# Kernel tuning notes

Measured on AMD Instinct MI355X. Metric: run time of the kernel, lower is better.

## Reference

```python
import jax, jax.numpy as jnp
import numpy as np

N_NODES = 100000
N_EDGES = 1600000
N_GRAPHS = 1024
F = 128
L = 3  # num_gnn_layers
EPS = 1e-5


def _ln(x, g, b):
    mu = jnp.mean(x, axis=-1, keepdims=True)
    v = jnp.mean((x - mu) ** 2, axis=-1, keepdims=True)
    return (x - mu) * jax.lax.rsqrt(v + EPS) * g + b


def setup_inputs() -> dict:
    key = jax.random.key(0)
    ks = jax.random.split(key, 40)
    s = 0.05
    d = {}
    d['x'] = jax.random.normal(ks[0], (N_NODES, F), jnp.float32)
    d['w'] = jax.random.uniform(ks[1], (N_NODES, 1), jnp.float32)
    d['edge_index'] = jax.random.randint(ks[2], (2, N_EDGES), 0, N_NODES)
    d['batch'] = jnp.sort(jax.random.randint(ks[3], (N_NODES,), 0, N_GRAPHS))
    # input linear: (monomer_features+1) -> gc_features
    d['W_in'] = jax.random.normal(ks[4], (F + 1, F), jnp.float32) * s
    d['b_in'] = jnp.zeros((F,), jnp.float32)
    # stacked GCBlock params [L, ...]
    d['sage_Wl'] = jax.random.normal(ks[5], (L, F, F), jnp.float32) * s
    d['sage_bl'] = jnp.zeros((L, F), jnp.float32)
    d['sage_Wr'] = jax.random.normal(ks[6], (L, F, F), jnp.float32) * s
    d['ln1_g'] = jnp.ones((L, F), jnp.float32)
    d['ln1_b'] = jnp.zeros((L, F), jnp.float32)
    d['lin1_W'] = jax.random.normal(ks[7], (L, F, F), jnp.float32) * s
    d['lin1_b'] = jnp.zeros((L, F), jnp.float32)
    d['lin2_W'] = jax.random.normal(ks[8], (L, F, F), jnp.float32) * s
    d['lin2_b'] = jnp.zeros((L, F), jnp.float32)
    d['ln2_g'] = jnp.ones((L, F), jnp.float32)
    d['ln2_b'] = jnp.zeros((L, F), jnp.float32)
    # MeanDiffFeatureBlock: Linear(2F -> F)
    d['mdf_W'] = jax.random.normal(ks[9], (2 * F, F), jnp.float32) * s
    d['mdf_b'] = jnp.zeros((F,), jnp.float32)
    # mean PoolingLayer params
    d['pln1_g'] = jnp.ones((F,), jnp.float32)
    d['pln1_b'] = jnp.zeros((F,), jnp.float32)
    d['plin1_W'] = jax.random.normal(ks[10], (F, F), jnp.float32) * s
    d['plin1_b'] = jnp.zeros((F,), jnp.float32)
    d['plin2_W'] = jax.random.normal(ks[11], (F, F), jnp.float32) * s
    d['plin2_b'] = jnp.zeros((F,), jnp.float32)
    d['pln2_g'] = jnp.ones((F,), jnp.float32)
    d['pln2_b'] = jnp.zeros((F,), jnp.float32)
    return d


def reference(x, w, edge_index, batch, W_in, b_in, sage_Wl, sage_bl, sage_Wr,
              ln1_g, ln1_b, lin1_W, lin1_b, lin2_W, lin2_b, ln2_g, ln2_b,
              mdf_W, mdf_b, pln1_g, pln1_b, plin1_W, plin1_b, plin2_W, plin2_b,
              pln2_g, pln2_b):
    src, dst = edge_index[0], edge_index[1]
    # in-degree for SAGE mean aggregation (clamped so isolated nodes -> 0 agg)
    deg = jax.ops.segment_sum(jnp.ones((N_EDGES,), jnp.float32), dst,
                              num_segments=N_NODES)
    deg = jnp.maximum(deg, 1.0)[:, None]
    # graph sizes for global_mean_pool
    cnt = jax.ops.segment_sum(jnp.ones((N_NODES,), jnp.float32), batch,
                              num_segments=N_GRAPHS)
    cnt = jnp.maximum(cnt, 1.0)[:, None]

    # inilinear on [x, weight-fraction]  (scalers are identity at init)
    h = jnp.concatenate([x, w], axis=-1) @ W_in + b_in  # [N, F]

    def gc_block(h, p):
        Wl, bl, Wr, g1, b1, W1, bb1, W2, bb2, g2, b2 = p
        # SAGEConv: lin_l(mean_j x_j) + lin_r(x_i)
        agg = jax.ops.segment_sum(h[src], dst, num_segments=N_NODES) / deg
        y = agg @ Wl + bl + h @ Wr
        y1 = _ln(y + h, g1, b1)
        y2 = jax.nn.elu(y1 @ W1 + bb1) @ W2 + bb2  # dropout = identity (eval)
        return _ln(y2 + y1, g2, b2), None

    h, _ = jax.lax.scan(gc_block, h,
                        (sage_Wl, sage_bl, sage_Wr, ln1_g, ln1_b,
                         lin1_W, lin1_b, lin2_W, lin2_b, ln2_g, ln2_b))

    # MeanDiffFeatureBlock
    gm = jax.ops.segment_sum(h, batch, num_segments=N_GRAPHS) / cnt  # [B, F]
    h = jnp.concatenate([h, h - gm[batch]], axis=-1) @ mdf_W + mdf_b

    # mean PoolingLayer
    p = jax.ops.segment_sum(h, batch, num_segments=N_GRAPHS) / cnt  # [B, F]
    hh = _ln(p, pln1_g, pln1_b)
    y = jax.nn.elu(hh @ plin1_W + plin1_b) @ plin2_W + plin2_b
    return _ln(y + hh, pln2_g, pln2_b)  # [B, F]
```

## Files before the change

### kernel.cpp

```cpp
#include <hip/hip_runtime.h>
#include <math.h>

#define NN 100000
#define NE 1600000
#define NG 1024
#define FF 128
#define BSH 9
#define NBK ((NN + 511) >> BSH)
#define RB 512
#define BCAP 16384

typedef __attribute__((ext_vector_type(8))) short short8;
typedef __attribute__((ext_vector_type(4))) float f32x4;
typedef __attribute__((ext_vector_type(2))) float f32x2;

__device__ __forceinline__ unsigned short f2b(float f) {
    union { float f; unsigned u; } v; v.f = f;
    unsigned r = (v.u + 0x7FFF + ((v.u >> 16) & 1)) >> 16;
    return (unsigned short)r;
}
__device__ __forceinline__ float us2f(unsigned short u) {
    union { unsigned u; float f; } v; v.u = ((unsigned)u) << 16; return v.f;
}
__device__ __forceinline__ float fast_elu(float v) {
    float e = __builtin_amdgcn_exp2f(v * 1.44269504088896340736f) - 1.0f;
    return v > 0.f ? v : e;
}
__device__ __forceinline__ uint2 pk8(const float* v) {
    unsigned lo = 0, hi = 0;
    lo = (unsigned)__builtin_amdgcn_cvt_pk_fp8_f32(v[0], v[1], (int)lo, false);
    lo = (unsigned)__builtin_amdgcn_cvt_pk_fp8_f32(v[2], v[3], (int)lo, true);
    hi = (unsigned)__builtin_amdgcn_cvt_pk_fp8_f32(v[4], v[5], (int)hi, false);
    hi = (unsigned)__builtin_amdgcn_cvt_pk_fp8_f32(v[6], v[7], (int)hi, true);
    uint2 r; r.x = lo; r.y = hi; return r;
}
#define MFMA(a, b, c) __builtin_amdgcn_mfma_f32_16x16x32_bf16((a), (b), (c), 0, 0, 0)

__global__ __launch_bounds__(256)
void radix_scatter(const int* __restrict__ src, const int* __restrict__ dst,
                   int* __restrict__ bcur, unsigned* __restrict__ pairs, int n) {
    __shared__ int base[NBK];
    __shared__ int cnt[NBK];
    for (int i = threadIdx.x; i < NBK; i += 256) cnt[i] = 0;
    __syncthreads();
    const int per = (((n + RB - 1) / RB) + 3) & ~3;
    const int beg = blockIdx.x * per;
    const int end = min(n, beg + per);
    {
        int i = beg + 4 * (int)threadIdx.x;
        for (; i + 3 < end; i += 1024) {
            int4 d4 = *(const int4*)&dst[i];
            atomicAdd(&cnt[d4.x >> BSH], 1);
            atomicAdd(&cnt[d4.y >> BSH], 1);
            atomicAdd(&cnt[d4.z >> BSH], 1);
            atomicAdd(&cnt[d4.w >> BSH], 1);
        }
        for (; i < end; ++i) atomicAdd(&cnt[dst[i] >> BSH], 1);
    }
    __syncthreads();
    for (int i = threadIdx.x; i < NBK; i += 256)
        base[i] = cnt[i] ? atomicAdd(&bcur[i], cnt[i]) : 0;
    __syncthreads();
    {
        int i = beg + 4 * (int)threadIdx.x;
        for (; i + 3 < end; i += 1024) {
            int4 d4 = *(const int4*)&dst[i];
            int4 s4 = *(const int4*)&src[i];
            int p;
            p = atomicAdd(&base[d4.x >> BSH], 1);
            pairs[p] = ((unsigned)s4.x << BSH) | (unsigned)(d4.x & 511);
            p = atomicAdd(&base[d4.y >> BSH], 1);
            pairs[p] = ((unsigned)s4.y << BSH) | (unsigned)(d4.y & 511);
            p = atomicAdd(&base[d4.z >> BSH], 1);
            pairs[p] = ((unsigned)s4.z << BSH) | (unsigned)(d4.z & 511);
            p = atomicAdd(&base[d4.w >> BSH], 1);
            pairs[p] = ((unsigned)s4.w << BSH) | (unsigned)(d4.w & 511);
        }
        for (; i < end; ++i) {
            int d = dst[i];
            int p = atomicAdd(&base[d >> BSH], 1);
            pairs[p] = ((unsigned)src[i] << BSH) | (unsigned)(d & 511);
        }
    }
}

__global__ __launch_bounds__(512)
void bucket_build(const unsigned* __restrict__ pairs, const int* __restrict__ bcur,
                  int* __restrict__ row_beg, int* __restrict__ row_end,
                  float* __restrict__ inv_deg, int* __restrict__ ssrc,
                  const int* __restrict__ batch, int* __restrict__ g_off,
                  float* __restrict__ inv_cnt) {
    __shared__ int cnt[512];
    __shared__ int curs[512];
    __shared__ int wsum[8];
    const int b = blockIdx.x;
    const int n0 = b << BSH;
    const int t = threadIdx.x;
    const int lane = t & 63, wid = t >> 6;

    {
        int g = b * 512 + t;
        if (g <= NG) {
            if (g == NG) {
                g_off[NG] = NN;
            } else {
                int lo = 0, hi = NN;
                while (lo < hi) { int mid = (lo + hi) >> 1; if (batch[mid] < g) lo = mid + 1; else hi = mid; }
                int lo2 = lo, hi2 = NN;
                while (lo2 < hi2) { int mid = (lo2 + hi2) >> 1; if (batch[mid] < g + 1) lo2 = mid + 1; else hi2 = mid; }
                g_off[g] = lo;
                int c = lo2 - lo;
                inv_cnt[g] = 1.0f / (float)(c > 1 ? c : 1);
            }
        }
    }

    cnt[t] = 0;
    __syncthreads();
    const int beg = b * BCAP, end = bcur[b];
    {
        int i = beg + 4 * t;
        for (; i + 3 < end; i += 2048) {
            uint4 p4 = *(const uint4*)&pairs[i];
            atomicAdd(&cnt[p4.x & 511], 1);
            atomicAdd(&cnt[p4.y & 511], 1);
            atomicAdd(&cnt[p4.z & 511], 1);
            atomicAdd(&cnt[p4.w & 511], 1);
        }
        for (; i < end; ++i) atomicAdd(&cnt[pairs[i] & 511], 1);
    }
    __syncthreads();

    int c = cnt[t];
    int x = c;
    #pragma unroll
    for (int o = 1; o < 64; o <<= 1) {
        int y = __shfl_up(x, o);
        if (lane >= o) x += y;
    }
    if (lane == 63) wsum[wid] = x;
    __syncthreads();
    if (t == 0) {
        int s = 0;
        #pragma unroll
        for (int w2 = 0; w2 < 8; ++w2) { int tv = wsum[w2]; wsum[w2] = s; s += tv; }
    }
    __syncthreads();
    int g0 = beg + wsum[wid] + x - c;
    curs[t] = g0;
    {
        int node = n0 + t;
        if (node < NN) {
            row_beg[node] = g0; row_end[node] = g0 + c;
            inv_deg[node] = 1.0f / (float)(c > 1 ? c : 1);
        }
    }
    __syncthreads();
    {
        int i = beg + 4 * t;
        for (; i + 3 < end; i += 2048) {
            uint4 p4 = *(const uint4*)&pairs[i];
            int p;
            p = atomicAdd(&curs[p4.x & 511], 1); ssrc[p] = (int)(p4.x >> BSH) << 7;
            p = atomicAdd(&curs[p4.y & 511], 1); ssrc[p] = (int)(p4.y >> BSH) << 7;
            p = atomicAdd(&curs[p4.z & 511], 1); ssrc[p] = (int)(p4.z >> BSH) << 7;
            p = atomicAdd(&curs[p4.w & 511], 1); ssrc[p] = (int)(p4.w >> BSH) << 7;
        }
        for (; i < end; ++i) {
            unsigned pr = pairs[i];
            int p = atomicAdd(&curs[pr & 511], 1);
            ssrc[p] = (int)(pr >> BSH) << 7;
        }
    }
}

struct WTab { const float* a[16]; };
__global__ __launch_bounds__(256)
void prep_weights(WTab tab, unsigned short* __restrict__ dst,
                  int* __restrict__ bcur, int* __restrict__ ssrc) {
    __shared__ unsigned short Wl[128 * 128];
    const int w = blockIdx.x;
    const int t = threadIdx.x;
    if (w == 0) {
        for (int i = t; i < NBK; i += 256) bcur[i] = i * BCAP;
        if (t == 0) ssrc[0] = 0;
    }
    const float4* src = (const float4*)tab.a[w];
    for (int i = t; i < 4096; i += 256) {
        float4 v = src[i];
        ushort4 o = {f2b(v.x), f2b(v.y), f2b(v.z), f2b(v.w)};
        *(ushort4*)&Wl[i * 4] = o;
    }
    __syncthreads();
    unsigned short* dw = dst + (size_t)w * 16384;
    for (int i2 = 0; i2 < 64; ++i2) {
        int idx = t + i2 * 256;
        int j = idx & 7, lane = (idx >> 3) & 63, nt = (idx >> 9) & 7, kc = idx >> 12;
        int cb = lane & 15, rq = lane >> 4;
        int k = kc * 32 + rq * 8 + j;
        int n = nt * 16 + cb;
        dw[idx] = Wl[k * 128 + n];
    }
}

__global__ __launch_bounds__(256)
void sage_agg(const unsigned char* __restrict__ h8, const int* __restrict__ row_beg,
              const int* __restrict__ row_end, const float* __restrict__ inv_deg,
              const int* __restrict__ ssrc, unsigned short* __restrict__ aggb) {
    const int wid = threadIdx.x >> 6;
    const int lane = threadIdx.x & 63;
    const int n0 = blockIdx.x * 8 + wid * 2;
    const int n1 = n0 + 1;
    const int eg = lane >> 4, j = lane & 15;
    const int jo = j * 8;
    const int beg0 = row_beg[n0], end0 = row_end[n0];
    const int beg1 = row_beg[n1], end1 = row_end[n1];
    f32x2 a0 = {0.f, 0.f}, a1 = {0.f, 0.f}, a2 = {0.f, 0.f}, a3 = {0.f, 0.f};
    f32x2 b0 = {0.f, 0.f}, b1 = {0.f, 0.f}, b2 = {0.f, 0.f}, b3 = {0.f, 0.f};
    int e0 = beg0 + eg, e1 = beg1 + eg;
    const int d0 = end0 - beg0, d1 = end1 - beg1;
    const int nit = ((d0 > d1 ? d0 : d1) + 31) >> 5;
    for (int it = 0; it < nit; ++it, e0 += 32, e1 += 32) {
        uint2 u0[8], u1[8];
        #pragma unroll
        for (int k = 0; k < 8; ++k) {
            int ek = e0 + 4 * k;
            bool ok = ek < end0;
            int idx = ssrc[ok ? ek : 0];
            uint2 uu = *(const uint2*)(h8 + (unsigned)(idx + jo));
            uu.x = ok ? uu.x : 0u;
            uu.y = ok ? uu.y : 0u;
            u0[k] = uu;
        }
        #pragma unroll
        for (int k = 0; k < 8; ++k) {
            int ek = e1 + 4 * k;
            bool ok = ek < end1;
            int idx = ssrc[ok ? ek : 0];
            uint2 uu = *(const uint2*)(h8 + (unsigned)(idx + jo));
            uu.x = ok ? uu.x : 0u;
            uu.y = ok ? uu.y : 0u;
            u1[k] = uu;
        }
        #pragma unroll
        for (int k = 0; k < 8; ++k) {
            a0 += __builtin_amdgcn_cvt_pk_f32_fp8(u0[k].x, false);
            a1 += __builtin_amdgcn_cvt_pk_f32_fp8(u0[k].x, true);
            a2 += __builtin_amdgcn_cvt_pk_f32_fp8(u0[k].y, false);
            a3 += __builtin_amdgcn_cvt_pk_f32_fp8(u0[k].y, true);
            b0 += __builtin_amdgcn_cvt_pk_f32_fp8(u1[k].x, false);
            b1 += __builtin_amdgcn_cvt_pk_f32_fp8(u1[k].x, true);
            b2 += __builtin_amdgcn_cvt_pk_f32_fp8(u1[k].y, false);
            b3 += __builtin_amdgcn_cvt_pk_f32_fp8(u1[k].y, true);
        }
    }
    float af[8] = {a0.x, a0.y, a1.x, a1.y, a2.x, a2.y, a3.x, a3.y};
    float bf[8] = {b0.x, b0.y, b1.x, b1.y, b2.x, b2.y, b3.x, b3.y};
    #pragma unroll
    for (int k = 0; k < 8; ++k) {
        af[k] += __shfl_xor(af[k], 16);
        af[k] += __shfl_xor(af[k], 32);
        bf[k] += __shfl_xor(bf[k], 16);
        bf[k] += __shfl_xor(bf[k], 32);
    }
    if (eg == 0) {
        float id0 = inv_deg[n0];
        float id1 = inv_deg[n1];
        #pragma unroll
        for (int nt = 0; nt < 8; ++nt) {
            aggb[(size_t)n0 * 128 + nt * 16 + j] = f2b(af[nt] * id0);
            aggb[(size_t)n1 * 128 + nt * 16 + j] = f2b(bf[nt] * id1);
        }
    }
}

__global__ __launch_bounds__(256)
void pool_mean_b(const unsigned short* __restrict__ src, const int* __restrict__ g_off,
                 const float* __restrict__ inv_cnt, float* __restrict__ out) {
    __shared__ float red[3][128];
    const int g = blockIdx.x;
    const int t = threadIdx.x;
    const int lane = t & 63, wid = t >> 6;
    const int j = lane & 15, rs = lane >> 4;
    const int beg = g_off[g], end = g_off[g + 1];
    float s[8] = {0.f, 0.f, 0.f, 0.f, 0.f, 0.f, 0.f, 0.f};
    for (int n = beg + rs + wid * 4; n < end; n += 16) {
        short8 v = *(const short8*)&src[(size_t)n * FF + j * 8];
        #pragma unroll
        for (int i = 0; i < 8; ++i) s[i] += us2f((unsigned short)v[i]);
    }
    #pragma unroll
    for (int i = 0; i < 8; ++i) {
        s[i] += __shfl_xor(s[i], 16);
        s[i] += __shfl_xor(s[i], 32);
    }
    if (wid > 0 && rs == 0) {
        #pragma unroll
        for (int i = 0; i < 8; ++i) red[wid - 1][j * 8 + i] = s[i];
    }
    __syncthreads();
    if (wid == 0 && rs == 0) {
        float ic = inv_cnt[g];
        #pragma unroll
        for (int i = 0; i < 8; ++i) {
            float v = s[i] + red[0][j * 8 + i] + red[1][j * 8 + i] + red[2][j * 8 + i];
            out[(size_t)g * FF + j * 8 + i] = v * ic;
        }
    }
}

template<bool AB16, bool R1, int RESM, int ACT, bool LN, bool OF32, bool OB16, bool OB8>
__global__ __launch_bounds__(256)
void gemm_mfma(const void* __restrict__ A_,
               const unsigned short* __restrict__ Wf,
               const float* __restrict__ bias,
               const float* __restrict__ rvec, const float* __restrict__ rrow,
               const float* __restrict__ res,
               const float* __restrict__ lng, const float* __restrict__ lnb,
               float* __restrict__ outf, unsigned short* __restrict__ outb,
               unsigned char* __restrict__ outb8, int M) {
    __shared__ short Al[64 * 136];

    const int t = threadIdx.x;
    const int lane = t & 63, wid = t >> 6;
    const int m0 = blockIdx.x * 64;
    const int cb = lane & 15, rq = lane >> 4;
    const int band = wid * 16;

    if (AB16) {
        const unsigned short* Ab = (const unsigned short*)A_;
        #pragma unroll
        for (int i2 = 0; i2 < 4; ++i2) {
            int i = lane + i2 * 64;
            int row = band + (i >> 4), seg = i & 15;
            int gr = m0 + row; if (gr >= M) gr = M - 1;
            *(uint4*)&Al[row * 136 + seg * 8] = *(const uint4*)&Ab[(size_t)gr * 128 + seg * 8];
        }
    } else {
        const float* Af = (const float*)A_;
        #pragma unroll
        for (int i2 = 0; i2 < 8; ++i2) {
            int i = lane + i2 * 64;
            int row = band + (i >> 5), seg = i & 31;
            int gr = m0 + row; if (gr >= M) gr = M - 1;
            float4 v = *(const float4*)&Af[(size_t)gr * 128 + seg * 4];
            ushort4 o = {f2b(v.x), f2b(v.y), f2b(v.z), f2b(v.w)};
            *(ushort4*)&Al[row * 136 + seg * 4] = o;
        }
    }

    f32x4 acc[8];
    #pragma unroll
    for (int nt = 0; nt < 8; ++nt) acc[nt] = (f32x4){0.f, 0.f, 0.f, 0.f};

    const int aoff_base = (band + cb) * 136 + rq * 8;
    for (int kc = 0; kc < 4; ++kc) {
        short8 a0 = *(const short8*)&Al[aoff_base + kc * 32];
        #pragma unroll
        for (int nt = 0; nt < 8; ++nt) {
            short8 b0 = *(const short8*)&Wf[(size_t)(kc * 8 + nt) * 512 + lane * 8];
            acc[nt] = MFMA(a0, b0, acc[nt]);
        }
    }

    float bs[8], rr[8], lg[8], lb[8];
    #pragma unroll
    for (int nt = 0; nt < 8; ++nt) {
        int col = nt * 16 + cb;
        bs[nt] = bias[col];
        if (R1) rr[nt] = rrow[col];
        if (LN) { lg[nt] = lng[col]; lb[nt] = lnb[col]; }
    }
    #pragma unroll
    for (int reg = 0; reg < 4; ++reg) {
        int m = m0 + band + rq * 4 + reg;
        int mc = m < M ? m : M - 1;
        float v[8];
        #pragma unroll
        for (int nt = 0; nt < 8; ++nt) v[nt] = acc[nt][reg] + bs[nt];
        if (R1) {
            float rv = rvec[mc];
            #pragma unroll
            for (int nt = 0; nt < 8; ++nt) v[nt] += rv * rr[nt];
        }
        if (RESM == 1) {
            #pragma unroll
            for (int nt = 0; nt < 8; ++nt) v[nt] += res[(size_t)mc * 128 + nt * 16 + cb];
        }
        if (ACT == 1) {
            #pragma unroll
            for (int nt = 0; nt < 8; ++nt) v[nt] = fast_elu(v[nt]);
        }
        if (LN) {
            float s1 = 0.f, s2 = 0.f;
            #pragma unroll
            for (int nt = 0; nt < 8; ++nt) { s1 += v[nt]; s2 += v[nt] * v[nt]; }
            #pragma unroll
            for (int o = 8; o >= 1; o >>= 1) { s1 += __shfl_xor(s1, o); s2 += __shfl_xor(s2, o); }
            float mu = s1 * (1.f / 128.f);
            float rs = rsqrtf(s2 * (1.f / 128.f) - mu * mu + 1e-5f);
            #pragma unroll
            for (int nt = 0; nt < 8; ++nt) v[nt] = (v[nt] - mu) * rs * lg[nt] + lb[nt];
        }
        if (m < M) {
            #pragma unroll
            for (int nt = 0; nt < 8; ++nt) {
                size_t o = (size_t)m * 128 + nt * 16 + cb;
                if (OF32) outf[o] = v[nt];
                if (OB16) outb[o] = f2b(v[nt]);
            }
            if (OB8) *(uint2*)&outb8[(size_t)m * 128 + cb * 8] = pk8(v);
        }
    }
}

__global__ __launch_bounds__(256)
void gc_chain(const unsigned short* __restrict__ hin, const unsigned short* __restrict__ aggb,
              unsigned short* __restrict__ hout, unsigned char* __restrict__ h8out,
              const unsigned short* __restrict__ Wl_f, const unsigned short* __restrict__ Wr_f,
              const unsigned short* __restrict__ W1_f, const unsigned short* __restrict__ W2_f,
              const float* __restrict__ bl,
              const float* __restrict__ g1, const float* __restrict__ b1,
              const float* __restrict__ bb1, const float* __restrict__ bb2,
              const float* __restrict__ g2, const float* __restrict__ b2, int M) {
    __shared__ short Hl[64 * 136];
    __shared__ short Gl[64 * 136];

    const int t = threadIdx.x;
    const int lane = t & 63, wid = t >> 6;
    const int m0 = blockIdx.x * 64;
    const int cb = lane & 15, rq = lane >> 4;
    const int band = wid * 16;
    const int aoff_base = (band + cb) * 136 + rq * 8;
    const int boff = lane * 8;

    #pragma unroll
    for (int i2 = 0; i2 < 4; ++i2) {
        int i = lane + i2 * 64;
        int row = band + (i >> 4), seg = i & 15;
        int gr = m0 + row; if (gr >= M) gr = M - 1;
        *(uint4*)&Hl[row * 136 + seg * 8] = *(const uint4*)&hin[(size_t)gr * 128 + seg * 8];
        *(uint4*)&Gl[row * 136 + seg * 8] = *(const uint4*)&aggb[(size_t)gr * 128 + seg * 8];
    }

    f32x4 acc[8];
    #pragma unroll
    for (int nt = 0; nt < 8; ++nt) acc[nt] = (f32x4){0.f, 0.f, 0.f, 0.f};

    for (int kc = 0; kc < 4; ++kc) {
        short8 a0 = *(const short8*)&Gl[aoff_base + kc * 32];
        short8 a1 = *(const short8*)&Hl[aoff_base + kc * 32];
        #pragma unroll
        for (int nt = 0; nt < 8; ++nt) {
            const size_t wo = (size_t)(kc * 8 + nt) * 512 + boff;
            acc[nt] = MFMA(a0, *(const short8*)&Wl_f[wo], acc[nt]);
            acc[nt] = MFMA(a1, *(const short8*)&Wr_f[wo], acc[nt]);
        }
    }

    float y1r[4][8];
    {
        float bs[8], lg[8], lb[8];
        #pragma unroll
        for (int nt = 0; nt < 8; ++nt) {
            int col = nt * 16 + cb;
            bs[nt] = bl[col]; lg[nt] = g1[col]; lb[nt] = b1[col];
        }
        #pragma unroll
        for (int reg = 0; reg < 4; ++reg) {
            int r = band + rq * 4 + reg;
            float v[8];
            float s1 = 0.f, s2 = 0.f;
            #pragma unroll
            for (int nt = 0; nt < 8; ++nt) {
                v[nt] = acc[nt][reg] + bs[nt] + us2f((unsigned short)Hl[r * 136 + nt * 16 + cb]);
                s1 += v[nt]; s2 += v[nt] * v[nt];
            }
            #pragma unroll
            for (int o = 8; o >= 1; o >>= 1) { s1 += __shfl_xor(s1, o); s2 += __shfl_xor(s2, o); }
            float mu = s1 * (1.f / 128.f);
            float rs = rsqrtf(s2 * (1.f / 128.f) - mu * mu + 1e-5f);
            #pragma unroll
            for (int nt = 0; nt < 8; ++nt) {
                float y = (v[nt] - mu) * rs * lg[nt] + lb[nt];
                y1r[reg][nt] = y;
                Hl[r * 136 + nt * 16 + cb] = (short)f2b(y);
            }
        }
    }

    #pragma unroll
    for (int nt = 0; nt < 8; ++nt) acc[nt] = (f32x4){0.f, 0.f, 0.f, 0.f};
    for (int kc = 0; kc < 4; ++kc) {
        short8 a0 = *(const short8*)&Hl[aoff_base + kc * 32];
        #pragma unroll
        for (int nt = 0; nt < 8; ++nt)
            acc[nt] = MFMA(a0, *(const short8*)&W1_f[(size_t)(kc * 8 + nt) * 512 + boff], acc[nt]);
    }
    {
        float bs[8];
        #pragma unroll
        for (int nt = 0; nt < 8; ++nt) bs[nt] = bb1[nt * 16 + cb];
        #pragma unroll
        for (int reg = 0; reg < 4; ++reg) {
            int r = band + rq * 4 + reg;
            #pragma unroll
            for (int nt = 0; nt < 8; ++nt) {
                float v = fast_elu(acc[nt][reg] + bs[nt]);
                Gl[r * 136 + nt * 16 + cb] = (short)f2b(v);
            }
        }
    }

    #pragma unroll
    for (int nt = 0; nt < 8; ++nt) acc[nt] = (f32x4){0.f, 0.f, 0.f, 0.f};
    for (int kc = 0; kc < 4; ++kc) {
        short8 a0 = *(const short8*)&Gl[aoff_base + kc * 32];
        #pragma unroll
        for (int nt = 0; nt < 8; ++nt)
            acc[nt] = MFMA(a0, *(const short8*)&W2_f[(size_t)(kc * 8 + nt) * 512 + boff], acc[nt]);
    }
    {
        float bs[8], lg[8], lb[8];
        #pragma unroll
        for (int nt = 0; nt < 8; ++nt) {
            int col = nt * 16 + cb;
            bs[nt] = bb2[col]; lg[nt] = g2[col]; lb[nt] = b2[col];
        }
        #pragma unroll
        for (int reg = 0; reg < 4; ++reg) {
            int r = band + rq * 4 + reg;
            int m = m0 + r;
            float v[8];
            float s1 = 0.f, s2 = 0.f;
            #pragma unroll
            for (int nt = 0; nt < 8; ++nt) {
                v[nt] = acc[nt][reg] + bs[nt] + y1r[reg][nt];
                s1 += v[nt]; s2 += v[nt] * v[nt];
            }
            #pragma unroll
            for (int o = 8; o >= 1; o >>= 1) { s1 += __shfl_xor(s1, o); s2 += __shfl_xor(s2, o); }
            float mu = s1 * (1.f / 128.f);
            float rs = rsqrtf(s2 * (1.f / 128.f) - mu * mu + 1e-5f);
            if (m < M) {
                float fv[8];
                #pragma unroll
                for (int nt = 0; nt < 8; ++nt) {
                    fv[nt] = (v[nt] - mu) * rs * lg[nt] + lb[nt];
                    hout[(size_t)m * 128 + nt * 16 + cb] = f2b(fv[nt]);
                }
                *(uint2*)&h8out[(size_t)m * 128 + cb * 8] = pk8(fv);
            }
        }
    }
}

__global__ __launch_bounds__(256)
void head_chain(const float* __restrict__ gm,
                const unsigned short* __restrict__ Wa_f,
                const unsigned short* __restrict__ P1_f,
                const unsigned short* __restrict__ P2_f,
                const float* __restrict__ mdfb,
                const float* __restrict__ g1, const float* __restrict__ b1,
                const float* __restrict__ p1b, const float* __restrict__ p2b,
                const float* __restrict__ g2, const float* __restrict__ b2,
                float* __restrict__ outp) {
    __shared__ short Al[64 * 136];

    const int t = threadIdx.x;
    const int lane = t & 63, wid = t >> 6;
    const int m0 = blockIdx.x * 64;
    const int cb = lane & 15, rq = lane >> 4;
    const int band = wid * 16;
    const int aoff_base = (band + cb) * 136 + rq * 8;
    const int boff = lane * 8;

    #pragma unroll
    for (int i2 = 0; i2 < 8; ++i2) {
        int i = lane + i2 * 64;
        int row = band + (i >> 5), seg = i & 31;
        float4 v = *(const float4*)&gm[(size_t)(m0 + row) * 128 + seg * 4];
        ushort4 o = {f2b(v.x), f2b(v.y), f2b(v.z), f2b(v.w)};
        *(ushort4*)&Al[row * 136 + seg * 4] = o;
    }

    f32x4 acc[8];
    #pragma unroll
    for (int nt = 0; nt < 8; ++nt) acc[nt] = (f32x4){0.f, 0.f, 0.f, 0.f};
    for (int kc = 0; kc < 4; ++kc) {
        short8 a0 = *(const short8*)&Al[aoff_base + kc * 32];
        #pragma unroll
        for (int nt = 0; nt < 8; ++nt)
            acc[nt] = MFMA(a0, *(const short8*)&Wa_f[(size_t)(kc * 8 + nt) * 512 + boff], acc[nt]);
    }
    float y1r[4][8];
    {
        float bs[8], lg[8], lb[8];
        #pragma unroll
        for (int nt = 0; nt < 8; ++nt) {
            int col = nt * 16 + cb;
            bs[nt] = mdfb[col]; lg[nt] = g1[col]; lb[nt] = b1[col];
        }
        #pragma unroll
        for (int reg = 0; reg < 4; ++reg) {
            int r = band + rq * 4 + reg;
            float v[8];
            float s1 = 0.f, s2 = 0.f;
            #pragma unroll
            for (int nt = 0; nt < 8; ++nt) {
                v[nt] = acc[nt][reg] + bs[nt];
                s1 += v[nt]; s2 += v[nt] * v[nt];
            }
            #pragma unroll
            for (int o = 8; o >= 1; o >>= 1) { s1 += __shfl_xor(s1, o); s2 += __shfl_xor(s2, o); }
            float mu = s1 * (1.f / 128.f);
            float rs = rsqrtf(s2 * (1.f / 128.f) - mu * mu + 1e-5f);
            #pragma unroll
            for (int nt = 0; nt < 8; ++nt) {
                float y = (v[nt] - mu) * rs * lg[nt] + lb[nt];
                y1r[reg][nt] = y;
                Al[r * 136 + nt * 16 + cb] = (short)f2b(y);
            }
        }
    }

    #pragma unroll
    for (int nt = 0; nt < 8; ++nt) acc[nt] = (f32x4){0.f, 0.f, 0.f, 0.f};
    for (int kc = 0; kc < 4; ++kc) {
        short8 a0 = *(const short8*)&Al[aoff_base + kc * 32];
        #pragma unroll
        for (int nt = 0; nt < 8; ++nt)
            acc[nt] = MFMA(a0, *(const short8*)&P1_f[(size_t)(kc * 8 + nt) * 512 + boff], acc[nt]);
    }
    {
        float bs[8];
        #pragma unroll
        for (int nt = 0; nt < 8; ++nt) bs[nt] = p1b[nt * 16 + cb];
        #pragma unroll
        for (int reg = 0; reg < 4; ++reg) {
            int r = band + rq * 4 + reg;
            #pragma unroll
            for (int nt = 0; nt < 8; ++nt) {
                float v = fast_elu(acc[nt][reg] + bs[nt]);
                Al[r * 136 + nt * 16 + cb] = (short)f2b(v);
            }
        }
    }

    #pragma unroll
    for (int nt = 0; nt < 8; ++nt) acc[nt] = (f32x4){0.f, 0.f, 0.f, 0.f};
    for (int kc = 0; kc < 4; ++kc) {
        short8 a0 = *(const short8*)&Al[aoff_base + kc * 32];
        #pragma unroll
        for (int nt = 0; nt < 8; ++nt)
            acc[nt] = MFMA(a0, *(const short8*)&P2_f[(size_t)(kc * 8 + nt) * 512 + boff], acc[nt]);
    }
    {
        float bs[8], lg[8], lb[8];
        #pragma unroll
        for (int nt = 0; nt < 8; ++nt) {
            int col = nt * 16 + cb;
            bs[nt] = p2b[col]; lg[nt] = g2[col]; lb[nt] = b2[col];
        }
        #pragma unroll
        for (int reg = 0; reg < 4; ++reg) {
            int r = band + rq * 4 + reg;
            int m = m0 + r;
            float v[8];
            float s1 = 0.f, s2 = 0.f;
            #pragma unroll
            for (int nt = 0; nt < 8; ++nt) {
                v[nt] = acc[nt][reg] + bs[nt] + y1r[reg][nt];
                s1 += v[nt]; s2 += v[nt] * v[nt];
            }
            #pragma unroll
            for (int o = 8; o >= 1; o >>= 1) { s1 += __shfl_xor(s1, o); s2 += __shfl_xor(s2, o); }
            float mu = s1 * (1.f / 128.f);
            float rs = rsqrtf(s2 * (1.f / 128.f) - mu * mu + 1e-5f);
            #pragma unroll
            for (int nt = 0; nt < 8; ++nt)
                outp[(size_t)m * 128 + nt * 16 + cb] = (v[nt] - mu) * rs * lg[nt] + lb[nt];
        }
    }
}

extern "C" void kernel_launch(void* const* d_in, const int* in_sizes, int n_in,
                              void* d_out, int out_size, void* d_ws, size_t ws_size,
                              hipStream_t stream) {
    const float* x      = (const float*)d_in[0];
    const float* w      = (const float*)d_in[1];
    const int*   ei     = (const int*)d_in[2];
    const int*   batch  = (const int*)d_in[3];
    const float* W_in   = (const float*)d_in[4];
    const float* b_in   = (const float*)d_in[5];
    const float* sage_Wl = (const float*)d_in[6];
    const float* sage_bl = (const float*)d_in[7];
    const float* sage_Wr = (const float*)d_in[8];
    const float* ln1_g  = (const float*)d_in[9];
    const float* ln1_b  = (const float*)d_in[10];
    const float* lin1_W = (const float*)d_in[11];
    const float* lin1_b = (const float*)d_in[12];
    const float* lin2_W = (const float*)d_in[13];
    const float* lin2_b = (const float*)d_in[14];
    const float* ln2_g  = (const float*)d_in[15];
    const float* ln2_b  = (const float*)d_in[16];
    const float* mdf_W  = (const float*)d_in[17];
    const float* mdf_b  = (const float*)d_in[18];
    const float* pln1_g = (const float*)d_in[19];
    const float* pln1_b = (const float*)d_in[20];
    const float* plin1_W = (const float*)d_in[21];
    const float* plin1_b = (const float*)d_in[22];
    const float* plin2_W = (const float*)d_in[23];
    const float* plin2_b = (const float*)d_in[24];
    const float* pln2_g = (const float*)d_in[25];
    const float* pln2_b = (const float*)d_in[26];
    float* out = (float*)d_out;

    const int* e_src = ei;
    const int* e_dst = ei + NE;

    float* ws = (float*)d_ws;
    size_t off = 0;
    float* gm    = ws + off; off += (size_t)NG * FF;
    float* inv_deg = ws + off; off += NN;
    float* inv_cnt = ws + off; off += NG;
    unsigned short* us = (unsigned short*)(ws + off);
    size_t uoff = 0;
    unsigned short* hb0  = us + uoff; uoff += (size_t)NN * FF;
    unsigned short* hb1  = us + uoff; uoff += (size_t)NN * FF;
    unsigned short* aggb = us + uoff; uoff += (size_t)NN * FF;
    unsigned short* wt   = us + uoff; uoff += (size_t)16 * 16384;
    int* iw = (int*)(us + uoff);
    size_t ioff = 0;
    unsigned* pairs = (unsigned*)iw; ioff += (size_t)NBK * BCAP;
    int* ssrc    = iw + ioff; ioff += (size_t)NBK * BCAP;
    int* row_beg = iw + ioff; ioff += NN;
    int* row_end = iw + ioff; ioff += NN;
    int* g_off   = iw + ioff; ioff += NG + 1;
    int* bcur    = iw + ioff; ioff += NBK;
    unsigned char* h8 = (unsigned char*)pairs;

    WTab tab;
    tab.a[0] = W_in;
    for (int l = 0; l < 3; ++l) {
        tab.a[1 + l]  = sage_Wl + (size_t)l * 16384;
        tab.a[4 + l]  = sage_Wr + (size_t)l * 16384;
        tab.a[7 + l]  = lin1_W + (size_t)l * 16384;
        tab.a[10 + l] = lin2_W + (size_t)l * 16384;
    }
    tab.a[13] = mdf_W;
    tab.a[14] = plin1_W;
    tab.a[15] = plin2_W;
    prep_weights<<<16, 256, 0, stream>>>(tab, wt, bcur, ssrc);
    const unsigned short* win_t = wt + 0 * 16384;
    const unsigned short* wa_t  = wt + 13 * 16384;
    const unsigned short* p1_t  = wt + 14 * 16384;
    const unsigned short* p2_t  = wt + 15 * 16384;

    radix_scatter<<<RB, 256, 0, stream>>>(e_src, e_dst, bcur, pairs, NE);
    bucket_build<<<NBK, 512, 0, stream>>>(pairs, bcur, row_beg, row_end,
                                          inv_deg, ssrc, batch, g_off, inv_cnt);

    const int GN = (NN + 63) / 64;
    const int GB = NG / 64;

    gemm_mfma<false, true, 0, 0, false, false, true, true><<<GN, 256, 0, stream>>>(
        x, win_t, b_in, w, W_in + 128 * 128,
        nullptr, nullptr, nullptr, nullptr, hb0, h8, NN);

    unsigned short* hcur = hb0;
    unsigned short* hnxt = hb1;
    for (int l = 0; l < 3; ++l) {
        sage_agg<<<NN / 8, 256, 0, stream>>>(h8, row_beg, row_end, inv_deg, ssrc, aggb);
        gc_chain<<<GN, 256, 0, stream>>>(
            hcur, aggb, hnxt, h8,
            wt + (size_t)(1 + l) * 16384, wt + (size_t)(4 + l) * 16384,
            wt + (size_t)(7 + l) * 16384, wt + (size_t)(10 + l) * 16384,
            sage_bl + (size_t)l * FF,
            ln1_g + (size_t)l * FF, ln1_b + (size_t)l * FF,
            lin1_b + (size_t)l * FF, lin2_b + (size_t)l * FF,
            ln2_g + (size_t)l * FF, ln2_b + (size_t)l * FF, NN);
        unsigned short* tmp = hcur; hcur = hnxt; hnxt = tmp;
    }

    pool_mean_b<<<NG, 256, 0, stream>>>(hcur, g_off, inv_cnt, gm);
    head_chain<<<GB, 256, 0, stream>>>(
        gm, wa_t, p1_t, p2_t, mdf_b,
        pln1_g, pln1_b, plin1_b, plin2_b, pln2_g, pln2_b, out);
}
```

Baseline: 488.0 us.

## Fuse edge radix scatter with input GEMM in one launch; update h in place

Merges the edge radix-scatter kernel and the input linear GEMM into a single launch. The first RB blocks do the scatter and the remaining blocks do the GEMM, so the two independent stages run concurrently and one launch is removed. The fp8 copy of h moves out of the pairs buffer into its own region, since pairs is now still being written while the GEMM writes h8. gc_chain also reads and writes the same bf16 h buffer in place, dropping the ping-pong buffer. This relies on each block touching only its own rows.

```diff
diff --git a/kernel.cpp b/kernel.cpp
--- a/kernel.cpp
+++ b/kernel.cpp
@@ -37,49 +37,113 @@
 #define MFMA(a, b, c) __builtin_amdgcn_mfma_f32_16x16x32_bf16((a), (b), (c), 0, 0, 0)
 
 __global__ __launch_bounds__(256)
-void radix_scatter(const int* __restrict__ src, const int* __restrict__ dst,
-                   int* __restrict__ bcur, unsigned* __restrict__ pairs, int n) {
-    __shared__ int base[NBK];
-    __shared__ int cnt[NBK];
-    for (int i = threadIdx.x; i < NBK; i += 256) cnt[i] = 0;
-    __syncthreads();
-    const int per = (((n + RB - 1) / RB) + 3) & ~3;
-    const int beg = blockIdx.x * per;
-    const int end = min(n, beg + per);
-    {
-        int i = beg + 4 * (int)threadIdx.x;
-        for (; i + 3 < end; i += 1024) {
-            int4 d4 = *(const int4*)&dst[i];
-            atomicAdd(&cnt[d4.x >> BSH], 1);
-            atomicAdd(&cnt[d4.y >> BSH], 1);
-            atomicAdd(&cnt[d4.z >> BSH], 1);
-            atomicAdd(&cnt[d4.w >> BSH], 1);
-        }
-        for (; i < end; ++i) atomicAdd(&cnt[dst[i] >> BSH], 1);
-    }
-    __syncthreads();
-    for (int i = threadIdx.x; i < NBK; i += 256)
-        base[i] = cnt[i] ? atomicAdd(&bcur[i], cnt[i]) : 0;
-    __syncthreads();
-    {
-        int i = beg + 4 * (int)threadIdx.x;
-        for (; i + 3 < end; i += 1024) {
-            int4 d4 = *(const int4*)&dst[i];
-            int4 s4 = *(const int4*)&src[i];
-            int p;
-            p = atomicAdd(&base[d4.x >> BSH], 1);
-            pairs[p] = ((unsigned)s4.x << BSH) | (unsigned)(d4.x & 511);
-            p = atomicAdd(&base[d4.y >> BSH], 1);
-            pairs[p] = ((unsigned)s4.y << BSH) | (unsigned)(d4.y & 511);
-            p = atomicAdd(&base[d4.z >> BSH], 1);
-            pairs[p] = ((unsigned)s4.z << BSH) | (unsigned)(d4.z & 511);
-            p = atomicAdd(&base[d4.w >> BSH], 1);
-            pairs[p] = ((unsigned)s4.w << BSH) | (unsigned)(d4.w & 511);
-        }
-        for (; i < end; ++i) {
-            int d = dst[i];
-            int p = atomicAdd(&base[d >> BSH], 1);
-            pairs[p] = ((unsigned)src[i] << BSH) | (unsigned)(d & 511);
+void scatter_gemm(const int* __restrict__ src, const int* __restrict__ dst,
+                  int* __restrict__ bcur, unsigned* __restrict__ pairs, int n,
+                  const float* __restrict__ x, const unsigned short* __restrict__ Wf,
+                  const float* __restrict__ bias,
+                  const float* __restrict__ rvec, const float* __restrict__ rrow,
+                  unsigned short* __restrict__ outb, unsigned char* __restrict__ outb8,
+                  int M) {
+    __shared__ short Al[64 * 136];
+
+    if (blockIdx.x < RB) {
+        int* cnt  = (int*)Al;
+        int* base = cnt + NBK;
+        for (int i = threadIdx.x; i < NBK; i += 256) cnt[i] = 0;
+        __syncthreads();
+        const int per = (((n + RB - 1) / RB) + 3) & ~3;
+        const int beg = blockIdx.x * per;
+        const int end = min(n, beg + per);
+        {
+            int i = beg + 4 * (int)threadIdx.x;
+            for (; i + 3 < end; i += 1024) {
+                int4 d4 = *(const int4*)&dst[i];
+                atomicAdd(&cnt[d4.x >> BSH], 1);
+                atomicAdd(&cnt[d4.y >> BSH], 1);
+                atomicAdd(&cnt[d4.z >> BSH], 1);
+                atomicAdd(&cnt[d4.w >> BSH], 1);
+            }
+            for (; i < end; ++i) atomicAdd(&cnt[dst[i] >> BSH], 1);
+        }
+        __syncthreads();
+        for (int i = threadIdx.x; i < NBK; i += 256)
+            base[i] = cnt[i] ? atomicAdd(&bcur[i], cnt[i]) : 0;
+        __syncthreads();
+        {
+            int i = beg + 4 * (int)threadIdx.x;
+            for (; i + 3 < end; i += 1024) {
+                int4 d4 = *(const int4*)&dst[i];
+                int4 s4 = *(const int4*)&src[i];
+                int p;
+                p = atomicAdd(&base[d4.x >> BSH], 1);
+                pairs[p] = ((unsigned)s4.x << BSH) | (unsigned)(d4.x & 511);
+                p = atomicAdd(&base[d4.y >> BSH], 1);
+                pairs[p] = ((unsigned)s4.y << BSH) | (unsigned)(d4.y & 511);
+                p = atomicAdd(&base[d4.z >> BSH], 1);
+                pairs[p] = ((unsigned)s4.z << BSH) | (unsigned)(d4.z & 511);
+                p = atomicAdd(&base[d4.w >> BSH], 1);
+                pairs[p] = ((unsigned)s4.w << BSH) | (unsigned)(d4.w & 511);
+            }
+            for (; i < end; ++i) {
+                int d = dst[i];
+                int p = atomicAdd(&base[d >> BSH], 1);
+                pairs[p] = ((unsigned)src[i] << BSH) | (unsigned)(d & 511);
+            }
+        }
+        return;
+    }
+
+    const int bid = blockIdx.x - RB;
+    const int t = threadIdx.x;
+    const int lane = t & 63, wid = t >> 6;
+    const int m0 = bid * 64;
+    const int cb = lane & 15, rq = lane >> 4;
+    const int band = wid * 16;
+
+    #pragma unroll
+    for (int i2 = 0; i2 < 8; ++i2) {
+        int i = lane + i2 * 64;
+        int row = band + (i >> 5), seg = i & 31;
+        int gr = m0 + row; if (gr >= M) gr = M - 1;
+        float4 v = *(const float4*)&x[(size_t)gr * 128 + seg * 4];
+        ushort4 o = {f2b(v.x), f2b(v.y), f2b(v.z), f2b(v.w)};
+        *(ushort4*)&Al[row * 136 + seg * 4] = o;
+    }
+
+    f32x4 acc[8];
+    #pragma unroll
+    for (int nt = 0; nt < 8; ++nt) acc[nt] = (f32x4){0.f, 0.f, 0.f, 0.f};
+
+    const int aoff_base = (band + cb) * 136 + rq * 8;
+    for (int kc = 0; kc < 4; ++kc) {
+        short8 a0 = *(const short8*)&Al[aoff_base + kc * 32];
+        #pragma unroll
+        for (int nt = 0; nt < 8; ++nt) {
+            short8 b0 = *(const short8*)&Wf[(size_t)(kc * 8 + nt) * 512 + lane * 8];
+            acc[nt] = MFMA(a0, b0, acc[nt]);
+        }
+    }
+
+    float bs[8], rr[8];
+    #pragma unroll
+    for (int nt = 0; nt < 8; ++nt) {
+        int col = nt * 16 + cb;
+        bs[nt] = bias[col];
+        rr[nt] = rrow[col];
+    }
+    #pragma unroll
+    for (int reg = 0; reg < 4; ++reg) {
+        int m = m0 + band + rq * 4 + reg;
+        int mc = m < M ? m : M - 1;
+        float v[8];
+        float rv = rvec[mc];
+        #pragma unroll
+        for (int nt = 0; nt < 8; ++nt) v[nt] = acc[nt][reg] + bs[nt] + rv * rr[nt];
+        if (m < M) {
+            #pragma unroll
+            for (int nt = 0; nt < 8; ++nt)
+                outb[(size_t)m * 128 + nt * 16 + cb] = f2b(v[nt]);
+            *(uint2*)&outb8[(size_t)m * 128 + cb * 8] = pk8(v);
         }
     }
 }
@@ -309,114 +373,9 @@
     }
 }
 
-template<bool AB16, bool R1, int RESM, int ACT, bool LN, bool OF32, bool OB16, bool OB8>
 __global__ __launch_bounds__(256)
-void gemm_mfma(const void* __restrict__ A_,
-               const unsigned short* __restrict__ Wf,
-               const float* __restrict__ bias,
-               const float* __restrict__ rvec, const float* __restrict__ rrow,
-               const float* __restrict__ res,
-               const float* __restrict__ lng, const float* __restrict__ lnb,
-               float* __restrict__ outf, unsigned short* __restrict__ outb,
-               unsigned char* __restrict__ outb8, int M) {
-    __shared__ short Al[64 * 136];
-
-    const int t = threadIdx.x;
-    const int lane = t & 63, wid = t >> 6;
-    const int m0 = blockIdx.x * 64;
-    const int cb = lane & 15, rq = lane >> 4;
-    const int band = wid * 16;
-
-    if (AB16) {
-        const unsigned short* Ab = (const unsigned short*)A_;
-        #pragma unroll
-        for (int i2 = 0; i2 < 4; ++i2) {
-            int i = lane + i2 * 64;
-            int row = band + (i >> 4), seg = i & 15;
-            int gr = m0 + row; if (gr >= M) gr = M - 1;
-            *(uint4*)&Al[row * 136 + seg * 8] = *(const uint4*)&Ab[(size_t)gr * 128 + seg * 8];
-        }
-    } else {
-        const float* Af = (const float*)A_;
-        #pragma unroll
-        for (int i2 = 0; i2 < 8; ++i2) {
-            int i = lane + i2 * 64;
-            int row = band + (i >> 5), seg = i & 31;
-            int gr = m0 + row; if (gr >= M) gr = M - 1;
-            float4 v = *(const float4*)&Af[(size_t)gr * 128 + seg * 4];
-            ushort4 o = {f2b(v.x), f2b(v.y), f2b(v.z), f2b(v.w)};
-            *(ushort4*)&Al[row * 136 + seg * 4] = o;
-        }
-    }
-
-    f32x4 acc[8];
-    #pragma unroll
-    for (int nt = 0; nt < 8; ++nt) acc[nt] = (f32x4){0.f, 0.f, 0.f, 0.f};
-
-    const int aoff_base = (band + cb) * 136 + rq * 8;
-    for (int kc = 0; kc < 4; ++kc) {
-        short8 a0 = *(const short8*)&Al[aoff_base + kc * 32];
-        #pragma unroll
-        for (int nt = 0; nt < 8; ++nt) {
-            short8 b0 = *(const short8*)&Wf[(size_t)(kc * 8 + nt) * 512 + lane * 8];
-            acc[nt] = MFMA(a0, b0, acc[nt]);
-        }
-    }
-
-    float bs[8], rr[8], lg[8], lb[8];
-    #pragma unroll
-    for (int nt = 0; nt < 8; ++nt) {
-        int col = nt * 16 + cb;
-        bs[nt] = bias[col];
-        if (R1) rr[nt] = rrow[col];
-        if (LN) { lg[nt] = lng[col]; lb[nt] = lnb[col]; }
-    }
-    #pragma unroll
-    for (int reg = 0; reg < 4; ++reg) {
-        int m = m0 + band + rq * 4 + reg;
-        int mc = m < M ? m : M - 1;
-        float v[8];
-        #pragma unroll
-        for (int nt = 0; nt < 8; ++nt) v[nt] = acc[nt][reg] + bs[nt];
-        if (R1) {
-            float rv = rvec[mc];
-            #pragma unroll
-            for (int nt = 0; nt < 8; ++nt) v[nt] += rv * rr[nt];
-        }
-        if (RESM == 1) {
-            #pragma unroll
-            for (int nt = 0; nt < 8; ++nt) v[nt] += res[(size_t)mc * 128 + nt * 16 + cb];
-        }
-        if (ACT == 1) {
-            #pragma unroll
-            for (int nt = 0; nt < 8; ++nt) v[nt] = fast_elu(v[nt]);
-        }
-        if (LN) {
-            float s1 = 0.f, s2 = 0.f;
-            #pragma unroll
-            for (int nt = 0; nt < 8; ++nt) { s1 += v[nt]; s2 += v[nt] * v[nt]; }
-            #pragma unroll
-            for (int o = 8; o >= 1; o >>= 1) { s1 += __shfl_xor(s1, o); s2 += __shfl_xor(s2, o); }
-            float mu = s1 * (1.f / 128.f);
-            float rs = rsqrtf(s2 * (1.f / 128.f) - mu * mu + 1e-5f);
-            #pragma unroll
-            for (int nt = 0; nt < 8; ++nt) v[nt] = (v[nt] - mu) * rs * lg[nt] + lb[nt];
-        }
-        if (m < M) {
-            #pragma unroll
-            for (int nt = 0; nt < 8; ++nt) {
-                size_t o = (size_t)m * 128 + nt * 16 + cb;
-                if (OF32) outf[o] = v[nt];
-                if (OB16) outb[o] = f2b(v[nt]);
-            }
-            if (OB8) *(uint2*)&outb8[(size_t)m * 128 + cb * 8] = pk8(v);
-        }
-    }
-}
-
-__global__ __launch_bounds__(256)
-void gc_chain(const unsigned short* __restrict__ hin, const unsigned short* __restrict__ aggb,
-              unsigned short* __restrict__ hout, unsigned char* __restrict__ h8out,
+void gc_chain(const unsigned short* hin, const unsigned short* __restrict__ aggb,
+              unsigned short* hout, unsigned char* __restrict__ h8out,
               const unsigned short* __restrict__ Wl_f, const unsigned short* __restrict__ Wr_f,
               const unsigned short* __restrict__ W1_f, const unsigned short* __restrict__ W2_f,
               const float* __restrict__ bl,
@@ -727,7 +686,6 @@
     unsigned short* us = (unsigned short*)(ws + off);
     size_t uoff = 0;
     unsigned short* hb0  = us + uoff; uoff += (size_t)NN * FF;
-    unsigned short* hb1  = us + uoff; uoff += (size_t)NN * FF;
     unsigned short* aggb = us + uoff; uoff += (size_t)NN * FF;
     unsigned short* wt   = us + uoff; uoff += (size_t)16 * 16384;
     int* iw = (int*)(us + uoff);
@@ -738,7 +696,7 @@
     int* row_end = iw + ioff; ioff += NN;
     int* g_off   = iw + ioff; ioff += NG + 1;
     int* bcur    = iw + ioff; ioff += NBK;
-    unsigned char* h8 = (unsigned char*)pairs;
+    unsigned char* h8 = (unsigned char*)(iw + ioff);
 
     WTab tab;
     tab.a[0] = W_in;
@@ -757,33 +715,29 @@
     const unsigned short* p1_t  = wt + 14 * 16384;
     const unsigned short* p2_t  = wt + 15 * 16384;
 
-    radix_scatter<<<RB, 256, 0, stream>>>(e_src, e_dst, bcur, pairs, NE);
+    const int GN = (NN + 63) / 64;
+    const int GB = NG / 64;
+
+    scatter_gemm<<<RB + GN, 256, 0, stream>>>(
+        e_src, e_dst, bcur, pairs, NE,
+        x, win_t, b_in, w, W_in + 128 * 128, hb0, h8, NN);
+
     bucket_build<<<NBK, 512, 0, stream>>>(pairs, bcur, row_beg, row_end,
                                           inv_deg, ssrc, batch, g_off, inv_cnt);
 
-    const int GN = (NN + 63) / 64;
-    const int GB = NG / 64;
-
-    gemm_mfma<false, true, 0, 0, false, false, true, true><<<GN, 256, 0, stream>>>(
-        x, win_t, b_in, w, W_in + 128 * 128,
-        nullptr, nullptr, nullptr, nullptr, hb0, h8, NN);
-
-    unsigned short* hcur = hb0;
-    unsigned short* hnxt = hb1;
     for (int l = 0; l < 3; ++l) {
         sage_agg<<<NN / 8, 256, 0, stream>>>(h8, row_beg, row_end, inv_deg, ssrc, aggb);
         gc_chain<<<GN, 256, 0, stream>>>(
-            hcur, aggb, hnxt, h8,
+            hb0, aggb, hb0, h8,
             wt + (size_t)(1 + l) * 16384, wt + (size_t)(4 + l) * 16384,
             wt + (size_t)(7 + l) * 16384, wt + (size_t)(10 + l) * 16384,
             sage_bl + (size_t)l * FF,
             ln1_g + (size_t)l * FF, ln1_b + (size_t)l * FF,
             lin1_b + (size_t)l * FF, lin2_b + (size_t)l * FF,
             ln2_g + (size_t)l * FF, ln2_b + (size_t)l * FF, NN);
-        unsigned short* tmp = hcur; hcur = hnxt; hnxt = tmp;
-    }
-
-    pool_mean_b<<<NG, 256, 0, stream>>>(hcur, g_off, inv_cnt, gm);
+    }
+
+    pool_mean_b<<<NG, 256, 0, stream>>>(hb0, g_off, inv_cnt, gm);
     head_chain<<<GB, 256, 0, stream>>>(
         gm, wa_t, p1_t, p2_t, mdf_b,
         pln1_g, pln1_b, plin1_b, plin2_b, pln2_g, pln2_b, out);
```

After: 508.6 us. 4.2% more time.
